# Optimization experiments

Hardware: AMD Instinct MI355X
Metric: run time of the kernel (lower is better)

Reference implementation:

```python
import jax, jax.numpy as jnp
import numpy as np

B, C, N, T = 32, 32, 512, 168
EMB = 40
K_NEI = 20
ALPHA = 3.0          # saturation rate in graph learning
GCN_DEPTH = 2
PROP_ALPHA = 0.05    # retaining ratio in mix-hop propagation
KERNELS = (2, 3, 6, 7)
DIL = 2
T_OUT = T - (max(KERNELS) - 1) * DIL   # 156
C_BR = C // len(KERNELS)               # 8 channels per inception branch
EPS = 1e-5


def _conv2d(x, w, b, dil):
    # x: (B,Cin,N,T), w: (Cout,Cin,1,k), temporal dilation dil
    y = jax.lax.conv_general_dilated(
        x, w, window_strides=(1, 1), padding='VALID',
        rhs_dilation=(1, dil), dimension_numbers=('NCHW', 'OIHW', 'NCHW'))
    return y + b[None, :, None, None]


def _inception(x, ws, bs):
    outs = [_conv2d(x, w, b, DIL) for w, b in zip(ws, bs)]
    tmin = outs[-1].shape[-1]   # largest kernel -> shortest output
    return jnp.concatenate([o[..., -tmin:] for o in outs], axis=1)


def setup_inputs() -> dict:
    key = jax.random.key(0)
    ks = jax.random.split(key, 32)
    d = {}
    d['x'] = jax.random.normal(ks[0], (B, C, N, T), jnp.float32)
    d['idx'] = jnp.arange(N)  # permutation of nodes (identity)
    # graph learning params
    d['emb1'] = jax.random.normal(ks[1], (N, EMB), jnp.float32)
    d['emb2'] = jax.random.normal(ks[2], (N, EMB), jnp.float32)
    d['W1'] = jax.random.normal(ks[3], (EMB, EMB), jnp.float32) * 0.15
    d['b1'] = jnp.zeros((EMB,), jnp.float32)
    d['W2'] = jax.random.normal(ks[4], (EMB, EMB), jnp.float32) * 0.15
    d['b2'] = jnp.zeros((EMB,), jnp.float32)
    # dilated inception filter/gate conv params
    i = 5
    for pre in ('f', 'g'):
        for k in KERNELS:
            d[f'{pre}w{k}'] = jax.random.normal(ks[i], (C_BR, C, 1, k), jnp.float32) * 0.05
            d[f'{pre}b{k}'] = jnp.zeros((C_BR,), jnp.float32)
            i += 1
    # mix-hop 1x1 mlp: (gcn_depth+1)*C -> C
    d['mlp_w'] = jax.random.normal(ks[i], (C, (GCN_DEPTH + 1) * C, 1, 1), jnp.float32) * 0.05
    d['mlp_b'] = jnp.zeros((C,), jnp.float32)
    # node-indexed layer norm affine params, shape (C, N, T_OUT)
    d['ln_w'] = jnp.ones((C, N, T_OUT), jnp.float32)
    d['ln_b'] = jnp.zeros((C, N, T_OUT), jnp.float32)
    return d


def reference(x, idx, emb1, emb2, W1, b1, W2, b2,
              fw2, fb2, fw3, fb3, fw6, fb6, fw7, fb7,
              gw2, gb2, gw3, gb3, gw6, gb6, gw7, gb7,
              mlp_w, mlp_b, ln_w, ln_b):
    # ---- graph learning: topk-masked adjacency (N,N) ----
    n1 = jnp.tanh(ALPHA * (emb1[idx] @ W1.T + b1))
    n2 = jnp.tanh(ALPHA * (emb2[idx] @ W2.T + b2))
    a = n1 @ n2.T - n2 @ n1.T
    A = jax.nn.relu(jnp.tanh(ALPHA * a))
    _, top_idx = jax.lax.top_k(A, K_NEI)                 # deterministic topk (torch adds rand*0.01 tiebreak)
    mask = jnp.zeros_like(A).at[jnp.arange(A.shape[0])[:, None], top_idx].set(1.0)
    A = A * mask

    # ---- dilated inception gated temporal conv ----
    filt = jnp.tanh(_inception(x, (fw2, fw3, fw6, fw7), (fb2, fb3, fb6, fb7)))
    gate = jax.nn.sigmoid(_inception(x, (gw2, gw3, gw6, gw7), (gb2, gb3, gb6, gb7)))
    z = filt * gate                                       # (B, C, N, T_OUT)

    # ---- mix-hop graph convolution ----
    Ah = A + jnp.eye(A.shape[0], dtype=A.dtype)
    Ah = Ah / Ah.sum(1, keepdims=True)                    # row-degree normalization
    h = z
    hops = [z]
    for _ in range(GCN_DEPTH):
        h = PROP_ALPHA * z + (1.0 - PROP_ALPHA) * jnp.einsum('bcwt,vw->bcvt', h, Ah)
        hops.append(h)
    h0 = jnp.concatenate(hops, axis=1)                    # (B, 3C, N, T_OUT)
    out = _conv2d(h0, mlp_w, mlp_b, 1)                    # 1x1 mlp -> (B, C, N, T_OUT)

    # ---- residual + node-indexed layer norm over dims (C,N,T) ----
    out = out + x[..., -T_OUT:]
    mean = out.mean(axis=(1, 2, 3), keepdims=True)
    var = out.var(axis=(1, 2, 3), keepdims=True)
    out = (out - mean) * jax.lax.rsqrt(var + EPS)
    out = out * ln_w[:, idx, :][None] + ln_b[:, idx, :][None]
    return out
```

## Files before the change

### kernel.cpp

```cpp
#include <hip/hip_runtime.h>

#define NB 32
#define NC 32
#define NNODE 512
#define NT 168
#define NTO 156
#define NQ 39
#define NEMB 40
#define KNEI 20
#define NADJ 21
#define ZT_PITCH 42
#define XROWS 176
#define NPB 4
#define CT (NC * NTO)
#define NPAIR (CT / 8)

static_assert(NTO == 4 * NQ, "t quads");

typedef __attribute__((ext_vector_type(8))) short bf16x8;
typedef __attribute__((ext_vector_type(16))) float f32x16;
typedef __attribute__((ext_vector_type(4))) float f32x4;
typedef __attribute__((ext_vector_type(8))) unsigned short u16x8;

__device__ __forceinline__ float fast_tanh(float x) {
  float e = __expf(2.0f * x);
  return 1.0f - 2.0f / (e + 1.0f);
}
__device__ __forceinline__ float fast_sigmoid(float x) {
  return 1.0f / (1.0f + __expf(-x));
}
__device__ __forceinline__ unsigned short f2b(float v) {
  unsigned int u = __float_as_uint(v);
  unsigned int r = (u + 0x7FFFu + ((u >> 16) & 1u)) >> 16;
  return (unsigned short)r;
}
__device__ __forceinline__ float b2f(unsigned short u) {
  return __uint_as_float((unsigned int)u << 16);
}
template <typename T>
__device__ __forceinline__ void pin(T& v) {
  f32x4 t = __builtin_bit_cast(f32x4, v);
  asm volatile("" : "+v"(t));
  v = __builtin_bit_cast(T, t);
}

__global__ __launch_bounds__(128) void g1_kernel(
    const float* __restrict__ emb1, const float* __restrict__ emb2,
    const float* __restrict__ W1, const float* __restrict__ b1,
    const float* __restrict__ W2, const float* __restrict__ b2,
    const int* __restrict__ idx, float* __restrict__ n1, float* __restrict__ n2) {
  const int v = blockIdx.x;
  const int tid = threadIdx.x;
  const int iv = idx[v];
  if (tid < NEMB) {
    float s = b1[tid];
    const float* er = emb1 + iv * NEMB;
    const float* wr = W1 + tid * NEMB;
    for (int f = 0; f < NEMB; ++f) s = fmaf(er[f], wr[f], s);
    n1[v * NEMB + tid] = tanhf(3.0f * s);
  } else if (tid >= 64 && tid < 64 + NEMB) {
    const int e = tid - 64;
    float s = b2[e];
    const float* er = emb2 + iv * NEMB;
    const float* wr = W2 + e * NEMB;
    for (int f = 0; f < NEMB; ++f) s = fmaf(er[f], wr[f], s);
    n2[v * NEMB + e] = tanhf(3.0f * s);
  }
}

__global__ __launch_bounds__(256) void g2_kernel(
    const float* __restrict__ n1, const float* __restrict__ n2,
    int* __restrict__ cols, float* __restrict__ wts) {
  const int v = blockIdx.x;
  const int tid = threadIdx.x;
  volatile __shared__ float Arow[NNODE];
  __shared__ float n1v[NEMB], n2v[NEMB];
  if (tid < NEMB) n1v[tid] = n1[v * NEMB + tid];
  if (tid >= 64 && tid < 64 + NEMB) n2v[tid - 64] = n2[v * NEMB + tid - 64];
  __syncthreads();
  for (int w = tid; w < NNODE; w += 256) {
    float d1 = 0.f, d2 = 0.f;
    const float* r1 = n1 + w * NEMB;
    const float* r2 = n2 + w * NEMB;
    for (int e = 0; e < NEMB; ++e) {
      d1 = fmaf(n1v[e], r2[e], d1);
      d2 = fmaf(n2v[e], r1[e], d2);
    }
    float a = tanhf(3.0f * (d1 - d2));
    Arow[w] = a > 0.f ? a : 0.f;
  }
  __syncthreads();
  if (tid >= 64) return;
  float sum = 1.0f;
  float selv[KNEI];
  int seli[KNEI];
  #pragma unroll
  for (int s = 0; s < KNEI; ++s) {
    float bv = -1.f; int bi = NNODE;
    #pragma unroll
    for (int w8 = 0; w8 < NNODE / 64; ++w8) {
      const int w = tid + 64 * w8;
      const float val = Arow[w];
      if (val > bv || (val == bv && w < bi)) { bv = val; bi = w; }
    }
    #pragma unroll
    for (int off = 32; off >= 1; off >>= 1) {
      const float ov = __shfl_down(bv, off);
      const int oi = __shfl_down(bi, off);
      if (ov > bv || (ov == bv && oi < bi)) { bv = ov; bi = oi; }
    }
    bv = __shfl(bv, 0);
    bi = __shfl(bi, 0);
    selv[s] = bv;
    seli[s] = bi;
    Arow[bi] = -2.f;
    sum += bv;
  }
  if (tid == 0) {
    const float inv = 1.0f / sum;
    #pragma unroll
    for (int s = 0; s < KNEI; ++s) {
      cols[v * NADJ + s] = seli[s];
      wts[v * NADJ + s] = selv[s] * inv;
    }
    cols[v * NADJ + KNEI] = v;
    wts[v * NADJ + KNEI] = inv;
  }
}

struct ZParams {
  const float* fw[4]; const float* fb[4];
  const float* gw[4]; const float* gb[4];
};

#define PA_CNT (2 * 2 * 7 * 64 * 8)
#define PB_CNT (2 * 64 * 16)
#define PNA_CNT (3 * 2 * 64 * 8)
__global__ __launch_bounds__(256) void pack_kernel(ZParams p, const float* __restrict__ mw,
                                                   unsigned short* __restrict__ pA,
                                                   float* __restrict__ pB,
                                                   unsigned short* __restrict__ pNA) {
  const int idx = blockIdx.x * 256 + threadIdx.x;
  if (idx < PA_CNT) {
    const int e = idx & 7;
    const int l = (idx >> 3) & 63;
    int rest = idx >> 9;
    const int j = rest % 7;
    rest /= 7;
    const int s = rest & 1;
    const int m = rest >> 1;
    const int row = l & 31;
    const int k = ((l >> 5) << 3) + e;
    const int ci = s * 16 + k;
    const int isF = (row < 16);
    const int co = m * 16 + (isF ? row : row - 16);
    const int br = co >> 3;
    const int kk = (br == 0) ? 2 : (br == 1) ? 3 : (br == 2) ? 6 : 7;
    const int jw = j - (7 - kk);
    const float* arr = isF ? p.fw[br] : p.gw[br];
    float val = (jw >= 0) ? arr[((co & 7) * NC + ci) * kk + jw] : 0.f;
    pA[idx] = f2b(val);
  } else if (idx < PA_CNT + PB_CNT) {
    const int ib = idx - PA_CNT;
    const int r = ib & 15;
    const int l = (ib >> 4) & 63;
    const int m = ib >> 10;
    const int rr = r & 7;
    const int row = (rr & 3) + 8 * (rr >> 2) + 4 * (l >> 5);
    const int co = m * 16 + row;
    const int br = co >> 3;
    const float* arr = (r < 8) ? p.fb[br] : p.gb[br];
    pB[ib] = arr[co & 7];
  } else if (idx < PA_CNT + PB_CNT + PNA_CNT) {
    const int in_ = idx - (PA_CNT + PB_CNT);
    const int e = in_ & 7;
    const int l = (in_ >> 3) & 63;
    const int s = (in_ >> 9) & 1;
    const int which = in_ >> 10;
    const int co = l & 31;
    const int c = s * 16 + ((l >> 5) << 3) + e;
    const float w0 = mw[co * 96 + c];
    const float w1 = mw[co * 96 + 32 + c];
    const float w2 = mw[co * 96 + 64 + c];
    float val;
    if (which == 0)      val = w0 + 0.05f * (w1 + w2);
    else if (which == 1) val = 0.95f * w1 + 0.0475f * w2;
    else                 val = 0.9025f * w2;
    pNA[in_] = f2b(val);
  }
}

__global__ __launch_bounds__(256) void xprep_kernel(
    const float* __restrict__ x, unsigned short* __restrict__ xbf) {
  const int n = blockIdx.x;
  const int b = blockIdx.y;
  const int tid = threadIdx.x;
  const int cp = tid & 15;
  const int t0 = tid >> 4;
  const float* xc0 = x + ((size_t)(b * NC + 2 * cp) * NNODE + n) * NT;
  const float* xc1 = xc0 + (size_t)NNODE * NT;
  unsigned int* dst = (unsigned int*)(xbf + (size_t)(b * NNODE + n) * (XROWS * NC));
  #pragma unroll
  for (int k = 0; k < 11; ++k) {
    const int t = t0 + 16 * k;
    unsigned int v = 0;
    if (t < NT) {
      v = (unsigned int)f2b(xc0[t]) | ((unsigned int)f2b(xc1[t]) << 16);
    }
    dst[t * 16 + cp] = v;
  }
}

__attribute__((amdgpu_waves_per_eu(2, 4)))
__global__ __launch_bounds__(256) void zs_kernel(
    const unsigned short* __restrict__ xbf, const unsigned short* __restrict__ pA,
    const float* __restrict__ pBias, const unsigned short* __restrict__ pNA,
    unsigned short* __restrict__ S) {
  __shared__ unsigned short zt[160 * ZT_PITCH];
  const int n0 = blockIdx.x * NPB;
  const int b = blockIdx.y;
  const int tid = threadIdx.x;
  if (tid < 4 * ZT_PITCH) zt[156 * ZT_PITCH + tid] = 0;
  const int w = tid >> 6, l = tid & 63;
  const int jc = l & 31, h = l >> 5;
  const int m = w & 1;

  bf16x8 aF[2][7];
  #pragma unroll
  for (int s = 0; s < 2; ++s)
    #pragma unroll
    for (int j = 0; j < 7; ++j) {
      aF[s][j] = *reinterpret_cast<const bf16x8*>(
          pA + ((((m * 2 + s) * 7 + j) << 6) + l) * 8);
      pin(aF[s][j]);
    }
  f32x4 bias4[4];
  {
    const f32x4* pb4 = reinterpret_cast<const f32x4*>(pBias + (m * 64 + l) * 16);
    #pragma unroll
    for (int q = 0; q < 4; ++q) { bias4[q] = pb4[q]; pin(bias4[q]); }
  }
  bf16x8 nA[3][2];
  #pragma unroll
  for (int which = 0; which < 3; ++which)
    #pragma unroll
    for (int s = 0; s < 2; ++s) {
      nA[which][s] = *reinterpret_cast<const bf16x8*>(
          pNA + (((which * 2 + s) << 6) + l) * 8);
      pin(nA[which][s]);
    }

  for (int nn = 0; nn < NPB; ++nn) {
    const int n = n0 + nn;
    const unsigned short* xbn = xbf + (size_t)(b * NNODE + n) * (XROWS * NC);
    for (int tile = (w >> 1); tile < 5; tile += 2) {
      const int t0 = tile * 32;
      f32x16 acc;
      #pragma unroll
      for (int r = 0; r < 16; ++r) acc[r] = bias4[r >> 2][r & 3];
      const unsigned short* bp = xbn + (t0 + jc) * NC + h * 8;
      #pragma unroll
      for (int j = 0; j < 7; ++j) {
        bf16x8 b0 = *reinterpret_cast<const bf16x8*>(bp + 2 * j * NC);
        bf16x8 b1 = *reinterpret_cast<const bf16x8*>(bp + 2 * j * NC + 16);
        acc = __builtin_amdgcn_mfma_f32_32x32x16_bf16(aF[0][j], b0, acc, 0, 0, 0);
        acc = __builtin_amdgcn_mfma_f32_32x32x16_bf16(aF[1][j], b1, acc, 0, 0, 0);
      }
      const int t = t0 + jc;
      if (t < NTO) {
        #pragma unroll
        for (int r = 0; r < 8; ++r) {
          const float f = fast_tanh(acc[r]);
          const float g = fast_sigmoid(acc[r + 8]);
          const int row = (r & 3) + 8 * (r >> 2) + 4 * h;
          const int co = m * 16 + row;
          zt[t * ZT_PITCH + co] = f2b(f * g);
        }
      }
    }
    __syncthreads();
    unsigned short* Sbv = S + (size_t)(b * NNODE + n) * 3 * CT;
    #pragma unroll
    for (int mat = 0; mat < 3; ++mat) {
      #pragma unroll
      for (int tile = 0; tile < 5; ++tile) {
        if (((mat * 5 + tile) & 3) != w) continue;
        const int t0 = tile * 32;
        const unsigned short* zp = zt + (t0 + jc) * ZT_PITCH + h * 8;
        bf16x8 b0 = *reinterpret_cast<const bf16x8*>(zp);
        bf16x8 b1 = *reinterpret_cast<const bf16x8*>(zp + 16);
        f32x16 d;
        #pragma unroll
        for (int r = 0; r < 16; ++r) d[r] = 0.f;
        d = __builtin_amdgcn_mfma_f32_32x32x16_bf16(nA[mat][0], b0, d, 0, 0, 0);
        d = __builtin_amdgcn_mfma_f32_32x32x16_bf16(nA[mat][1], b1, d, 0, 0, 0);
        const int t = t0 + jc;
        if (t < NTO) {
          unsigned short* so = Sbv + (size_t)mat * CT + (size_t)(4 * h) * NTO + t;
          #pragma unroll
          for (int r = 0; r < 16; ++r) {
            const int row = (r & 3) + 8 * (r >> 2);
            so[row * NTO] = f2b(d[r]);
          }
        }
      }
    }
    __syncthreads();
  }
}

__global__ __launch_bounds__(256) void m_kernel(
    const unsigned short* __restrict__ S, const int* __restrict__ cols,
    const float* __restrict__ wts, unsigned short* __restrict__ M) {
  const int bid = blockIdx.x;
  const int v = bid & (NNODE - 1);
  const int b = bid >> 9;
  const int tid = threadIdx.x;
  float acc[3][8];
  const unsigned short* s1p = S + ((size_t)bid * 3 + 1) * CT;
  #pragma unroll
  for (int k = 0; k < 2; ++k) {
    u16x8 u = *reinterpret_cast<const u16x8*>(s1p + 8 * (tid + 256 * k));
    #pragma unroll
    for (int j = 0; j < 8; ++j) acc[k][j] = b2f(u[j]);
  }
  if (tid < NPAIR - 512) {
    u16x8 u = *reinterpret_cast<const u16x8*>(s1p + 8 * (tid + 512));
    #pragma unroll
    for (int j = 0; j < 8; ++j) acc[2][j] = b2f(u[j]);
  }
  for (int s = 0; s < NADJ; ++s) {
    const int col = cols[v * NADJ + s];
    const float w = wts[v * NADJ + s];
    const unsigned short* p = S + (((size_t)(b << 9) + col) * 3 + 2) * CT;
    #pragma unroll
    for (int k = 0; k < 2; ++k) {
      u16x8 u = *reinterpret_cast<const u16x8*>(p + 8 * (tid + 256 * k));
      #pragma unroll
      for (int j = 0; j < 8; ++j) acc[k][j] = fmaf(w, b2f(u[j]), acc[k][j]);
    }
    if (tid < NPAIR - 512) {
      u16x8 u = *reinterpret_cast<const u16x8*>(p + 8 * (tid + 512));
      #pragma unroll
      for (int j = 0; j < 8; ++j) acc[2][j] = fmaf(w, b2f(u[j]), acc[2][j]);
    }
  }
  unsigned short* mp = M + (size_t)bid * CT;
  #pragma unroll
  for (int k = 0; k < 2; ++k) {
    u16x8 o;
    #pragma unroll
    for (int j = 0; j < 8; ++j) o[j] = f2b(acc[k][j]);
    *reinterpret_cast<u16x8*>(mp + 8 * (tid + 256 * k)) = o;
  }
  if (tid < NPAIR - 512) {
    u16x8 o;
    #pragma unroll
    for (int j = 0; j < 8; ++j) o[j] = f2b(acc[2][j]);
    *reinterpret_cast<u16x8*>(mp + 8 * (tid + 512)) = o;
  }
}

__global__ __launch_bounds__(256) void f_kernel(
    const unsigned short* __restrict__ S, const unsigned short* __restrict__ M,
    const float* __restrict__ x, const int* __restrict__ cols,
    const float* __restrict__ wts, const float* __restrict__ mb,
    unsigned short* __restrict__ P, float* __restrict__ stats) {
  const int bid = blockIdx.x;
  const int v = bid & (NNODE - 1);
  const int b = bid >> 9;
  const int tid = threadIdx.x;
  __shared__ float mbs[NC];
  if (tid < NC) mbs[tid] = mb[tid];
  float acc[3][8];
  const unsigned short* s0p = S + (size_t)bid * 3 * CT;
  #pragma unroll
  for (int k = 0; k < 2; ++k) {
    u16x8 u = *reinterpret_cast<const u16x8*>(s0p + 8 * (tid + 256 * k));
    #pragma unroll
    for (int j = 0; j < 8; ++j) acc[k][j] = b2f(u[j]);
  }
  if (tid < NPAIR - 512) {
    u16x8 u = *reinterpret_cast<const u16x8*>(s0p + 8 * (tid + 512));
    #pragma unroll
    for (int j = 0; j < 8; ++j) acc[2][j] = b2f(u[j]);
  }
  for (int s = 0; s < NADJ; ++s) {
    const int col = cols[v * NADJ + s];
    const float w = wts[v * NADJ + s];
    const unsigned short* p = M + ((size_t)(b << 9) + col) * CT;
    #pragma unroll
    for (int k = 0; k < 2; ++k) {
      u16x8 u = *reinterpret_cast<const u16x8*>(p + 8 * (tid + 256 * k));
      #pragma unroll
      for (int j = 0; j < 8; ++j) acc[k][j] = fmaf(w, b2f(u[j]), acc[k][j]);
    }
    if (tid < NPAIR - 512) {
      u16x8 u = *reinterpret_cast<const u16x8*>(p + 8 * (tid + 512));
      #pragma unroll
      for (int j = 0; j < 8; ++j) acc[2][j] = fmaf(w, b2f(u[j]), acc[2][j]);
    }
  }
  __syncthreads();
  float st1 = 0.f, st2 = 0.f;
  #pragma unroll
  for (int k = 0; k < 3; ++k) {
    const int pi = tid + 256 * k;
    if (pi < NPAIR) {
      #pragma unroll
      for (int hh = 0; hh < 2; ++hh) {
        const int e = 8 * pi + 4 * hh;
        const int c = e / NTO;
        const int t = e - c * NTO;
        const float bias = mbs[c];
        const size_t rowb = ((size_t)(b * NC + c) * NNODE + v);
        const float4 xr = *reinterpret_cast<const float4*>(x + rowb * NT + 12 + t);
        float4 o;
        o.x = acc[k][4 * hh + 0] + bias + xr.x;
        o.y = acc[k][4 * hh + 1] + bias + xr.y;
        o.z = acc[k][4 * hh + 2] + bias + xr.z;
        o.w = acc[k][4 * hh + 3] + bias + xr.w;
        ushort4 o4;
        o4.x = f2b(o.x); o4.y = f2b(o.y); o4.z = f2b(o.z); o4.w = f2b(o.w);
        *reinterpret_cast<ushort4*>(P + rowb * NTO + t) = o4;
        st1 += o.x + o.y + o.z + o.w;
        st2 += o.x * o.x + o.y * o.y + o.z * o.z + o.w * o.w;
      }
    }
  }
  #pragma unroll
  for (int off = 32; off >= 1; off >>= 1) {
    st1 += __shfl_down(st1, off);
    st2 += __shfl_down(st2, off);
  }
  __shared__ float r1[4], r2[4];
  const int lane = threadIdx.x & 63, wv_ = threadIdx.x >> 6;
  if (lane == 0) { r1[wv_] = st1; r2[wv_] = st2; }
  __syncthreads();
  if (threadIdx.x == 0) {
    atomicAdd(&stats[b * 2], r1[0] + r1[1] + r1[2] + r1[3]);
    atomicAdd(&stats[b * 2 + 1], r2[0] + r2[1] + r2[2] + r2[3]);
  }
}

__global__ __launch_bounds__(256) void ln_kernel(
    const unsigned short* __restrict__ P, float* __restrict__ out,
    const float* __restrict__ lnw, const float* __restrict__ lnb,
    const int* __restrict__ idx, const float* __restrict__ stats) {
  const int i = blockIdx.x * 256 + threadIdx.x;
  const int q = i % NQ;
  const int r = i / NQ;
  const int v = r % NNODE;
  const int r2 = r / NNODE;
  const int co = r2 % NC;
  const int b = r2 / NC;
  const float invM = 1.0f / (float)(NC * NNODE * NTO);
  const float mean = stats[b * 2] * invM;
  const float var = stats[b * 2 + 1] * invM - mean * mean;
  const float rs = rsqrtf(var + 1e-5f);
  ushort4 u = *reinterpret_cast<const ushort4*>(P + 4 * i);
  const int iv = idx[v];
  const int lb = (co * NNODE + iv) * NTO + 4 * q;
  const float4 w = *reinterpret_cast<const float4*>(lnw + lb);
  const float4 bb = *reinterpret_cast<const float4*>(lnb + lb);
  float4 o;
  o.x = (b2f(u.x) - mean) * rs * w.x + bb.x;
  o.y = (b2f(u.y) - mean) * rs * w.y + bb.y;
  o.z = (b2f(u.z) - mean) * rs * w.z + bb.z;
  o.w = (b2f(u.w) - mean) * rs * w.w + bb.w;
  *reinterpret_cast<float4*>(out + 4 * i) = o;
}

extern "C" void kernel_launch(void* const* d_in, const int* in_sizes, int n_in,
                              void* d_out, int out_size, void* d_ws, size_t ws_size,
                              hipStream_t stream) {
  const float* x    = (const float*)d_in[0];
  const int*   idx  = (const int*)d_in[1];
  const float* emb1 = (const float*)d_in[2];
  const float* emb2 = (const float*)d_in[3];
  const float* W1   = (const float*)d_in[4];
  const float* b1   = (const float*)d_in[5];
  const float* W2   = (const float*)d_in[6];
  const float* b2   = (const float*)d_in[7];
  const float* mlp_w = (const float*)d_in[24];
  const float* mlp_b = (const float*)d_in[25];
  const float* ln_w = (const float*)d_in[26];
  const float* ln_b = (const float*)d_in[27];

  char* ws = (char*)d_ws;
  float* n1    = (float*)(ws);
  float* n2    = (float*)(ws + (128 << 10));
  int*   cols  = (int*)  (ws + (256 << 10));
  float* wts   = (float*)(ws + (320 << 10));
  float* stats = (float*)(ws + (384 << 10));
  unsigned short* pA = (unsigned short*)(ws + (400 << 10));
  float* pBias = (float*)(ws + (440 << 10));
  unsigned short* pNA = (unsigned short*)(ws + (456 << 10));
  unsigned short* xbf = (unsigned short*)(ws + (512 << 10));
  const size_t xbf_elems = (size_t)NB * NNODE * XROWS * NC;
  unsigned short* S = xbf + xbf_elems;
  const size_t s_elems = (size_t)NB * NNODE * 3 * CT;
  unsigned short* M = S + s_elems;
  unsigned short* P = xbf;

  ZParams zp;
  for (int k = 0; k < 4; ++k) {
    zp.fw[k] = (const float*)d_in[8 + 2 * k];
    zp.fb[k] = (const float*)d_in[9 + 2 * k];
    zp.gw[k] = (const float*)d_in[16 + 2 * k];
    zp.gb[k] = (const float*)d_in[17 + 2 * k];
  }

  hipMemsetAsync(stats, 0, 2 * NB * sizeof(float), stream);
  g1_kernel<<<NNODE, 128, 0, stream>>>(emb1, emb2, W1, b1, W2, b2, idx, n1, n2);
  g2_kernel<<<NNODE, 256, 0, stream>>>(n1, n2, cols, wts);
  pack_kernel<<<76, 256, 0, stream>>>(zp, mlp_w, pA, pBias, pNA);
  xprep_kernel<<<dim3(NNODE, NB), 256, 0, stream>>>(x, xbf);
  zs_kernel<<<dim3(NNODE / NPB, NB), 256, 0, stream>>>(xbf, pA, pBias, pNA, S);
  m_kernel<<<NB * NNODE, 256, 0, stream>>>(S, cols, wts, M);
  f_kernel<<<NB * NNODE, 256, 0, stream>>>(S, M, x, cols, wts, mlp_b, P, stats);
  ln_kernel<<<NB * NC * NNODE * NQ / 256, 256, 0, stream>>>(P, (float*)d_out, ln_w,
                                                            ln_b, idx, stats);
}
```

Baseline: 1.389 ms.

## Propagate raw z through graph hops, apply mix-hop MLP afterwards with MFMA

The 1x1 mix-hop projection is now applied after propagation instead of before. Previously the code projected z into three channel slabs and evaluated W0 z + A(W1 z + A W2 z) in Horner form. Now a conv kernel writes only z, one shared hop kernel runs twice to build A z and A A z, and a new fin kernel applies the three packed weight matrices with MFMA, then adds bias and the residual and accumulates the layer-norm statistics. The aim is to drop the large scattered three-slab store from the conv kernel and replace it with a single contiguous slab write. In exchange it writes and reads an extra intermediate slab, and the new intermediate layout forces scattered residual loads from x in fin and reindexed output stores in the layer-norm kernel.

After: 1.378 ms. About the same (-0.8%).

```diff
diff --git a/kernel.cpp b/kernel.cpp
--- a/kernel.cpp
+++ b/kernel.cpp
@@ -211,16 +211,14 @@
   }
 }
 
-__attribute__((amdgpu_waves_per_eu(2, 4)))
-__global__ __launch_bounds__(256) void zs_kernel(
+__attribute__((amdgpu_waves_per_eu(2)))
+__global__ __launch_bounds__(256) void conv_kernel(
     const unsigned short* __restrict__ xbf, const unsigned short* __restrict__ pA,
-    const float* __restrict__ pBias, const unsigned short* __restrict__ pNA,
-    unsigned short* __restrict__ S) {
-  __shared__ unsigned short zt[160 * ZT_PITCH];
+    const float* __restrict__ pBias, unsigned short* __restrict__ z) {
+  __shared__ unsigned short zt[NTO * ZT_PITCH];
   const int n0 = blockIdx.x * NPB;
   const int b = blockIdx.y;
   const int tid = threadIdx.x;
-  if (tid < 4 * ZT_PITCH) zt[156 * ZT_PITCH + tid] = 0;
   const int w = tid >> 6, l = tid & 63;
   const int jc = l & 31, h = l >> 5;
   const int m = w & 1;
@@ -240,15 +238,6 @@
     #pragma unroll
     for (int q = 0; q < 4; ++q) { bias4[q] = pb4[q]; pin(bias4[q]); }
   }
-  bf16x8 nA[3][2];
-  #pragma unroll
-  for (int which = 0; which < 3; ++which)
-    #pragma unroll
-    for (int s = 0; s < 2; ++s) {
-      nA[which][s] = *reinterpret_cast<const bf16x8*>(
-          pNA + (((which * 2 + s) << 6) + l) * 8);
-      pin(nA[which][s]);
-    }
 
   for (int nn = 0; nn < NPB; ++nn) {
     const int n = n0 + nn;
@@ -279,60 +268,32 @@
       }
     }
     __syncthreads();
-    unsigned short* Sbv = S + (size_t)(b * NNODE + n) * 3 * CT;
-    #pragma unroll
-    for (int mat = 0; mat < 3; ++mat) {
-      #pragma unroll
-      for (int tile = 0; tile < 5; ++tile) {
-        if (((mat * 5 + tile) & 3) != w) continue;
-        const int t0 = tile * 32;
-        const unsigned short* zp = zt + (t0 + jc) * ZT_PITCH + h * 8;
-        bf16x8 b0 = *reinterpret_cast<const bf16x8*>(zp);
-        bf16x8 b1 = *reinterpret_cast<const bf16x8*>(zp + 16);
-        f32x16 d;
-        #pragma unroll
-        for (int r = 0; r < 16; ++r) d[r] = 0.f;
-        d = __builtin_amdgcn_mfma_f32_32x32x16_bf16(nA[mat][0], b0, d, 0, 0, 0);
-        d = __builtin_amdgcn_mfma_f32_32x32x16_bf16(nA[mat][1], b1, d, 0, 0, 0);
-        const int t = t0 + jc;
-        if (t < NTO) {
-          unsigned short* so = Sbv + (size_t)mat * CT + (size_t)(4 * h) * NTO + t;
-          #pragma unroll
-          for (int r = 0; r < 16; ++r) {
-            const int row = (r & 3) + 8 * (r >> 2);
-            so[row * NTO] = f2b(d[r]);
-          }
-        }
-      }
+    unsigned short* zv = z + (size_t)(b * NNODE + n) * CT;
+    for (int i = tid; i < CT / 4; i += 256) {
+      const int row = i >> 3, q = i & 7;
+      ushort4 v4 = *reinterpret_cast<const ushort4*>(zt + row * ZT_PITCH + 4 * q);
+      *reinterpret_cast<ushort4*>(zv + 4 * i) = v4;
     }
     __syncthreads();
   }
 }
 
-__global__ __launch_bounds__(256) void m_kernel(
-    const unsigned short* __restrict__ S, const int* __restrict__ cols,
-    const float* __restrict__ wts, unsigned short* __restrict__ M) {
+__global__ __launch_bounds__(256) void hop_kernel(
+    const unsigned short* __restrict__ src, const int* __restrict__ cols,
+    const float* __restrict__ wts, unsigned short* __restrict__ dst) {
   const int bid = blockIdx.x;
   const int v = bid & (NNODE - 1);
   const int b = bid >> 9;
   const int tid = threadIdx.x;
   float acc[3][8];
-  const unsigned short* s1p = S + ((size_t)bid * 3 + 1) * CT;
-  #pragma unroll
-  for (int k = 0; k < 2; ++k) {
-    u16x8 u = *reinterpret_cast<const u16x8*>(s1p + 8 * (tid + 256 * k));
-    #pragma unroll
-    for (int j = 0; j < 8; ++j) acc[k][j] = b2f(u[j]);
-  }
-  if (tid < NPAIR - 512) {
-    u16x8 u = *reinterpret_cast<const u16x8*>(s1p + 8 * (tid + 512));
-    #pragma unroll
-    for (int j = 0; j < 8; ++j) acc[2][j] = b2f(u[j]);
-  }
+  #pragma unroll
+  for (int k = 0; k < 3; ++k)
+    #pragma unroll
+    for (int j = 0; j < 8; ++j) acc[k][j] = 0.f;
   for (int s = 0; s < NADJ; ++s) {
     const int col = cols[v * NADJ + s];
     const float w = wts[v * NADJ + s];
-    const unsigned short* p = S + (((size_t)(b << 9) + col) * 3 + 2) * CT;
+    const unsigned short* p = src + ((size_t)(b << 9) + col) * CT;
     #pragma unroll
     for (int k = 0; k < 2; ++k) {
       u16x8 u = *reinterpret_cast<const u16x8*>(p + 8 * (tid + 256 * k));
@@ -345,86 +306,90 @@
       for (int j = 0; j < 8; ++j) acc[2][j] = fmaf(w, b2f(u[j]), acc[2][j]);
     }
   }
-  unsigned short* mp = M + (size_t)bid * CT;
+  unsigned short* dp = dst + ((size_t)(b << 9) + v) * CT;
   #pragma unroll
   for (int k = 0; k < 2; ++k) {
     u16x8 o;
     #pragma unroll
     for (int j = 0; j < 8; ++j) o[j] = f2b(acc[k][j]);
-    *reinterpret_cast<u16x8*>(mp + 8 * (tid + 256 * k)) = o;
+    *reinterpret_cast<u16x8*>(dp + 8 * (tid + 256 * k)) = o;
   }
   if (tid < NPAIR - 512) {
     u16x8 o;
     #pragma unroll
     for (int j = 0; j < 8; ++j) o[j] = f2b(acc[2][j]);
-    *reinterpret_cast<u16x8*>(mp + 8 * (tid + 512)) = o;
-  }
-}
-
-__global__ __launch_bounds__(256) void f_kernel(
-    const unsigned short* __restrict__ S, const unsigned short* __restrict__ M,
-    const float* __restrict__ x, const int* __restrict__ cols,
-    const float* __restrict__ wts, const float* __restrict__ mb,
+    *reinterpret_cast<u16x8*>(dp + 8 * (tid + 512)) = o;
+  }
+}
+
+__global__ __launch_bounds__(256) void fin_kernel(
+    const unsigned short* __restrict__ z, const unsigned short* __restrict__ g1,
+    const unsigned short* __restrict__ g2, const float* __restrict__ x,
+    const unsigned short* __restrict__ pNA, const float* __restrict__ mb,
     unsigned short* __restrict__ P, float* __restrict__ stats) {
-  const int bid = blockIdx.x;
-  const int v = bid & (NNODE - 1);
-  const int b = bid >> 9;
-  const int tid = threadIdx.x;
-  __shared__ float mbs[NC];
-  if (tid < NC) mbs[tid] = mb[tid];
-  float acc[3][8];
-  const unsigned short* s0p = S + (size_t)bid * 3 * CT;
-  #pragma unroll
-  for (int k = 0; k < 2; ++k) {
-    u16x8 u = *reinterpret_cast<const u16x8*>(s0p + 8 * (tid + 256 * k));
-    #pragma unroll
-    for (int j = 0; j < 8; ++j) acc[k][j] = b2f(u[j]);
-  }
-  if (tid < NPAIR - 512) {
-    u16x8 u = *reinterpret_cast<const u16x8*>(s0p + 8 * (tid + 512));
-    #pragma unroll
-    for (int j = 0; j < 8; ++j) acc[2][j] = b2f(u[j]);
-  }
-  for (int s = 0; s < NADJ; ++s) {
-    const int col = cols[v * NADJ + s];
-    const float w = wts[v * NADJ + s];
-    const unsigned short* p = M + ((size_t)(b << 9) + col) * CT;
-    #pragma unroll
-    for (int k = 0; k < 2; ++k) {
-      u16x8 u = *reinterpret_cast<const u16x8*>(p + 8 * (tid + 256 * k));
+  const int b = blockIdx.y;
+  const int tid = threadIdx.x;
+  const int w = tid >> 6, l = tid & 63;
+  const int jc = l & 31, h = l >> 5;
+  const int v = blockIdx.x * 4 + w;
+
+  bf16x8 nA[3][2];
+  #pragma unroll
+  for (int which = 0; which < 3; ++which)
+    #pragma unroll
+    for (int s = 0; s < 2; ++s) {
+      nA[which][s] = *reinterpret_cast<const bf16x8*>(
+          pNA + (((which * 2 + s) << 6) + l) * 8);
+      pin(nA[which][s]);
+    }
+  float mbr[16];
+  #pragma unroll
+  for (int r = 0; r < 16; ++r) {
+    const int co = (r & 3) + 8 * (r >> 2) + 4 * h;
+    mbr[r] = mb[co];
+  }
+
+  const size_t base = (size_t)(b << 9) + v;
+  const unsigned short* zs_ = z + base * CT;
+  const unsigned short* g1s = g1 + base * CT;
+  const unsigned short* g2s = g2 + base * CT;
+  unsigned short* Ps = P + base * CT;
+  float st1 = 0.f, st2 = 0.f;
+
+  #pragma unroll
+  for (int tile = 0; tile < 5; ++tile) {
+    const int t = tile * 32 + jc;
+    const int off = t * NC + h * 8;
+    f32x16 acc;
+    #pragma unroll
+    for (int r = 0; r < 16; ++r) acc[r] = 0.f;
+    {
+      bf16x8 b0 = *reinterpret_cast<const bf16x8*>(zs_ + off);
+      bf16x8 b1 = *reinterpret_cast<const bf16x8*>(zs_ + off + 16);
+      acc = __builtin_amdgcn_mfma_f32_32x32x16_bf16(nA[0][0], b0, acc, 0, 0, 0);
+      acc = __builtin_amdgcn_mfma_f32_32x32x16_bf16(nA[0][1], b1, acc, 0, 0, 0);
+    }
+    {
+      bf16x8 b0 = *reinterpret_cast<const bf16x8*>(g1s + off);
+      bf16x8 b1 = *reinterpret_cast<const bf16x8*>(g1s + off + 16);
+      acc = __builtin_amdgcn_mfma_f32_32x32x16_bf16(nA[1][0], b0, acc, 0, 0, 0);
+      acc = __builtin_amdgcn_mfma_f32_32x32x16_bf16(nA[1][1], b1, acc, 0, 0, 0);
+    }
+    {
+      bf16x8 b0 = *reinterpret_cast<const bf16x8*>(g2s + off);
+      bf16x8 b1 = *reinterpret_cast<const bf16x8*>(g2s + off + 16);
+      acc = __builtin_amdgcn_mfma_f32_32x32x16_bf16(nA[2][0], b0, acc, 0, 0, 0);
+      acc = __builtin_amdgcn_mfma_f32_32x32x16_bf16(nA[2][1], b1, acc, 0, 0, 0);
+    }
+    if (t < NTO) {
       #pragma unroll
-      for (int j = 0; j < 8; ++j) acc[k][j] = fmaf(w, b2f(u[j]), acc[k][j]);
-    }
-    if (tid < NPAIR - 512) {
-      u16x8 u = *reinterpret_cast<const u16x8*>(p + 8 * (tid + 512));
-      #pragma unroll
-      for (int j = 0; j < 8; ++j) acc[2][j] = fmaf(w, b2f(u[j]), acc[2][j]);
-    }
-  }
-  __syncthreads();
-  float st1 = 0.f, st2 = 0.f;
-  #pragma unroll
-  for (int k = 0; k < 3; ++k) {
-    const int pi = tid + 256 * k;
-    if (pi < NPAIR) {
-      #pragma unroll
-      for (int hh = 0; hh < 2; ++hh) {
-        const int e = 8 * pi + 4 * hh;
-        const int c = e / NTO;
-        const int t = e - c * NTO;
-        const float bias = mbs[c];
-        const size_t rowb = ((size_t)(b * NC + c) * NNODE + v);
-        const float4 xr = *reinterpret_cast<const float4*>(x + rowb * NT + 12 + t);
-        float4 o;
-        o.x = acc[k][4 * hh + 0] + bias + xr.x;
-        o.y = acc[k][4 * hh + 1] + bias + xr.y;
-        o.z = acc[k][4 * hh + 2] + bias + xr.z;
-        o.w = acc[k][4 * hh + 3] + bias + xr.w;
-        ushort4 o4;
-        o4.x = f2b(o.x); o4.y = f2b(o.y); o4.z = f2b(o.z); o4.w = f2b(o.w);
-        *reinterpret_cast<ushort4*>(P + rowb * NTO + t) = o4;
-        st1 += o.x + o.y + o.z + o.w;
-        st2 += o.x * o.x + o.y * o.y + o.z * o.z + o.w * o.w;
+      for (int r = 0; r < 16; ++r) {
+        const int co = (r & 3) + 8 * (r >> 2) + 4 * h;
+        const float xr = x[((size_t)(b * NC + co) * NNODE + v) * NT + 12 + t];
+        const float val = acc[r] + mbr[r] + xr;
+        Ps[co * NTO + t] = f2b(val);
+        st1 += val;
+        st2 += val * val;
       }
     }
   }
@@ -434,10 +399,9 @@
     st2 += __shfl_down(st2, off);
   }
   __shared__ float r1[4], r2[4];
-  const int lane = threadIdx.x & 63, wv_ = threadIdx.x >> 6;
-  if (lane == 0) { r1[wv_] = st1; r2[wv_] = st2; }
+  if ((tid & 63) == 0) { r1[w] = st1; r2[w] = st2; }
   __syncthreads();
-  if (threadIdx.x == 0) {
+  if (tid == 0) {
     atomicAdd(&stats[b * 2], r1[0] + r1[1] + r1[2] + r1[3]);
     atomicAdd(&stats[b * 2 + 1], r2[0] + r2[1] + r2[2] + r2[3]);
   }
@@ -450,10 +414,10 @@
   const int i = blockIdx.x * 256 + threadIdx.x;
   const int q = i % NQ;
   const int r = i / NQ;
-  const int v = r % NNODE;
-  const int r2 = r / NNODE;
-  const int co = r2 % NC;
-  const int b = r2 / NC;
+  const int co = r % NC;
+  const int r2 = r / NC;
+  const int v = r2 % NNODE;
+  const int b = r2 / NNODE;
   const float invM = 1.0f / (float)(NC * NNODE * NTO);
   const float mean = stats[b * 2] * invM;
   const float var = stats[b * 2 + 1] * invM - mean * mean;
@@ -468,7 +432,8 @@
   o.y = (b2f(u.y) - mean) * rs * w.y + bb.y;
   o.z = (b2f(u.z) - mean) * rs * w.z + bb.z;
   o.w = (b2f(u.w) - mean) * rs * w.w + bb.w;
-  *reinterpret_cast<float4*>(out + 4 * i) = o;
+  const int ob = ((b * NC + co) * NNODE + v) * NTO + 4 * q;
+  *reinterpret_cast<float4*>(out + ob) = o;
 }
 
 extern "C" void kernel_launch(void* const* d_in, const int* in_sizes, int n_in,
@@ -498,10 +463,11 @@
   unsigned short* pNA = (unsigned short*)(ws + (456 << 10));
   unsigned short* xbf = (unsigned short*)(ws + (512 << 10));
   const size_t xbf_elems = (size_t)NB * NNODE * XROWS * NC;
-  unsigned short* S = xbf + xbf_elems;
-  const size_t s_elems = (size_t)NB * NNODE * 3 * CT;
-  unsigned short* M = S + s_elems;
-  unsigned short* P = xbf;
+  const size_t slab_elems = (size_t)NB * NNODE * CT;
+  unsigned short* z  = xbf + xbf_elems;
+  unsigned short* g1 = z + slab_elems;
+  unsigned short* g2 = g1 + slab_elems;
+  unsigned short* P  = xbf;
 
   ZParams zp;
   for (int k = 0; k < 4; ++k) {
@@ -516,9 +482,11 @@
   g2_kernel<<<NNODE, 256, 0, stream>>>(n1, n2, cols, wts);
   pack_kernel<<<76, 256, 0, stream>>>(zp, mlp_w, pA, pBias, pNA);
   xprep_kernel<<<dim3(NNODE, NB), 256, 0, stream>>>(x, xbf);
-  zs_kernel<<<dim3(NNODE / NPB, NB), 256, 0, stream>>>(xbf, pA, pBias, pNA, S);
-  m_kernel<<<NB * NNODE, 256, 0, stream>>>(S, cols, wts, M);
-  f_kernel<<<NB * NNODE, 256, 0, stream>>>(S, M, x, cols, wts, mlp_b, P, stats);
+  conv_kernel<<<dim3(NNODE / NPB, NB), 256, 0, stream>>>(xbf, pA, pBias, z);
+  hop_kernel<<<NB * NNODE, 256, 0, stream>>>(z, cols, wts, g1);
+  hop_kernel<<<NB * NNODE, 256, 0, stream>>>(g1, cols, wts, g2);
+  fin_kernel<<<dim3(NNODE / 4, NB), 256, 0, stream>>>(z, g1, g2, x, pNA, mlp_b,
+                                                      P, stats);
   ln_kernel<<<NB * NC * NNODE * NQ / 256, 256, 0, stream>>>(P, (float*)d_out, ln_w,
                                                             ln_b, idx, stats);
 }
```
